# Kernel tuning notes

Measured on AMD Instinct MI355X. Metric: run time of the kernel, lower is better.

The kernel has to match this reference:

```python
import jax, jax.numpy as jnp
import numpy as np

EMBED_DIM = 128
HIDDEN_DIM = 512
NUM_LAYERS = 2
LATENT_DIM = 128
VOCAB = 2048
BATCH = 4096
NEG = -1.0e9  # matches torch masked fill value -1e9
TEMPERATURE = 1.0  # generate() skips the divide when temperature == 1.0


def _gru_cell(x, h, w_ih, w_hh, b_ih, b_hh):
    # PyTorch GRU cell, gate order (r, z, n)
    gi = x @ w_ih.T + b_ih          # [B, 3H]
    gh = h @ w_hh.T + b_hh          # [B, 3H]
    i_r, i_z, i_n = jnp.split(gi, 3, axis=-1)
    h_r, h_z, h_n = jnp.split(gh, 3, axis=-1)
    r = jax.nn.sigmoid(i_r + h_r)
    u = jax.nn.sigmoid(i_z + h_z)
    n = jnp.tanh(i_n + r * h_n)
    return (1.0 - u) * n + u * h


def setup_inputs() -> dict:
    key = jax.random.key(0)
    ks = jax.random.split(key, 16)

    def unif(k, shape, fan):
        bound = 1.0 / np.sqrt(fan)
        return jax.random.uniform(k, shape, jnp.float32, -bound, bound)

    embed = jax.random.normal(ks[0], (VOCAB, EMBED_DIM), jnp.float32)
    embed = embed.at[0].set(0.0)  # padding_idx = 0

    return dict(
        z=jax.random.normal(ks[1], (BATCH, LATENT_DIM), jnp.float32),
        embed=embed,
        w_lh=unif(ks[2], (NUM_LAYERS * HIDDEN_DIM, LATENT_DIM), LATENT_DIM),
        b_lh=unif(ks[3], (NUM_LAYERS * HIDDEN_DIM,), LATENT_DIM),
        w_ih0=unif(ks[4], (3 * HIDDEN_DIM, EMBED_DIM), HIDDEN_DIM),
        w_hh0=unif(ks[5], (3 * HIDDEN_DIM, HIDDEN_DIM), HIDDEN_DIM),
        b_ih0=unif(ks[6], (3 * HIDDEN_DIM,), HIDDEN_DIM),
        b_hh0=unif(ks[7], (3 * HIDDEN_DIM,), HIDDEN_DIM),
        w_ih1=unif(ks[8], (3 * HIDDEN_DIM, HIDDEN_DIM), HIDDEN_DIM),
        w_hh1=unif(ks[9], (3 * HIDDEN_DIM, HIDDEN_DIM), HIDDEN_DIM),
        b_ih1=unif(ks[10], (3 * HIDDEN_DIM,), HIDDEN_DIM),
        b_hh1=unif(ks[11], (3 * HIDDEN_DIM,), HIDDEN_DIM),
        w_out=unif(ks[12], (VOCAB, HIDDEN_DIM), HIDDEN_DIM),
        b_out=unif(ks[13], (VOCAB,), HIDDEN_DIM),
        bos_idx=1, eos_idx=2, pad_idx=0,
        max_len=64, top_k=40, min_generation_length=20,
    )


def reference(z, embed, w_lh, b_lh, w_ih0, w_hh0, b_ih0, b_hh0,
              w_ih1, w_hh1, b_ih1, b_hh1, w_out, b_out,
              bos_idx, eos_idx, pad_idx, max_len, top_k, min_generation_length):
    B = z.shape[0]
    V = w_out.shape[0]
    H = w_hh0.shape[1]
    eff_min = max(0, min(int(min_generation_length), max(0, max_len - 2)))

    # latent -> initial hidden state [L, B, H]
    h = jnp.tanh(z @ w_lh.T + b_lh).reshape(B, NUM_LAYERS, H).transpose(1, 0, 2)
    rows = jnp.arange(B)[:, None]

    def step(carry, t):
        h, cur, finished, key = carry
        key, sk = jax.random.split(key)
        x = embed[cur]                                   # [B, E]
        h0 = _gru_cell(x, h[0], w_ih0, w_hh0, b_ih0, b_hh0)
        h1 = _gru_cell(h0, h[1], w_ih1, w_hh1, b_ih1, b_hh1)
        logits = h1 @ w_out.T + b_out                    # [B, V]
        logits = logits.at[:, bos_idx].set(NEG).at[:, pad_idx].set(NEG)
        # block EOS until min_generation_length real tokens emitted
        logits = jnp.where((t - 1) < eff_min, logits.at[:, eos_idx].set(NEG), logits)
        if TEMPERATURE != 1.0:
            logits = logits / max(TEMPERATURE, 1e-6)
        if 0 < top_k < V:
            tv, ti = jax.lax.top_k(logits, top_k)
            logits = jnp.full_like(logits, NEG).at[rows, ti].set(tv)
        # multinomial over softmax(logits) == categorical on logits
        nxt = jax.random.categorical(sk, logits).astype(jnp.int32)
        nxt = jnp.where(finished, pad_idx, nxt)
        finished = finished | (nxt == eos_idx)
        return (jnp.stack([h0, h1]), nxt, finished, key), nxt

    init = (h,
            jnp.full((B,), bos_idx, jnp.int32),
            jnp.zeros((B,), dtype=bool),
            jax.random.key(1))
    _, toks = jax.lax.scan(step, init, jnp.arange(1, max_len))  # toks: [max_len-1, B]
    return jnp.concatenate(
        [jnp.full((B, 1), bos_idx, jnp.int32), toks.T.astype(jnp.int32)], axis=1)
```

## Files before the change

kernel.cpp:

```cpp
#include <hip/hip_runtime.h>
#include <cstdint>
#include <cstddef>

#ifndef PARTITIONABLE
#define PARTITIONABLE 1
#endif

namespace {
constexpr int kBatch  = 4096;
constexpr int kEmb    = 128;
constexpr int kHid    = 512;
constexpr int kVoc    = 2048;
constexpr int kMaxLen = 64;
constexpr int kTopK   = 40;
constexpr int kBos = 1, kEos = 2, kPad = 0;
constexpr int kEffMin = 20;
constexpr float kNeg  = -1.0e9f;
constexpr float kTiny = 1.17549435082228751e-38f;
}

typedef __bf16 bf16x8 __attribute__((ext_vector_type(8)));
typedef float  f32x4  __attribute__((ext_vector_type(4)));

__host__ __device__ inline void tf2x32(uint32_t k0, uint32_t k1,
                                       uint32_t x0, uint32_t x1,
                                       uint32_t& o0, uint32_t& o1) {
  uint32_t ks0 = k0, ks1 = k1, ks2 = k0 ^ k1 ^ 0x1BD11BDAu;
  x0 += ks0; x1 += ks1;
#define TFR(r) { x0 += x1; x1 = (x1 << (r)) | (x1 >> (32 - (r))); x1 ^= x0; }
  TFR(13) TFR(15) TFR(26) TFR(6)   x0 += ks1; x1 += ks2 + 1u;
  TFR(17) TFR(29) TFR(16) TFR(24)  x0 += ks2; x1 += ks0 + 2u;
  TFR(13) TFR(15) TFR(26) TFR(6)   x0 += ks0; x1 += ks1 + 3u;
  TFR(17) TFR(29) TFR(16) TFR(24)  x0 += ks1; x1 += ks2 + 4u;
  TFR(13) TFR(15) TFR(26) TFR(6)   x0 += ks2; x1 += ks0 + 5u;
#undef TFR
  o0 = x0; o1 = x1;
}

__device__ __forceinline__ float xla_tanh(float x) {
  float ax = fabsf(x);
  float xc = fminf(fmaxf(x, -9.0f), 9.0f);
  float x2 = __fmul_rn(xc, xc);
  float num = -2.76076847742355e-16f;
  num = __fadd_rn(__fmul_rn(x2, num), 2.00018790482477e-13f);
  num = __fadd_rn(__fmul_rn(x2, num), -8.60467152213735e-11f);
  num = __fadd_rn(__fmul_rn(x2, num), 5.12229709037114e-08f);
  num = __fadd_rn(__fmul_rn(x2, num), 1.48572235717979e-05f);
  num = __fadd_rn(__fmul_rn(x2, num), 6.37261928875436e-04f);
  num = __fadd_rn(__fmul_rn(x2, num), 4.89352455891786e-03f);
  num = __fmul_rn(xc, num);
  float den = 1.19825839466702e-06f;
  den = __fadd_rn(__fmul_rn(x2, den), 1.18534705686654e-04f);
  den = __fadd_rn(__fmul_rn(x2, den), 2.26843463243900e-03f);
  den = __fadd_rn(__fmul_rn(x2, den), 4.89352518554385e-03f);
  return (ax < 4.0e-04f) ? x : __fdiv_rn(num, den);
}

__device__ __forceinline__ float xla_sigmoid(float x) {
  return __fdiv_rn(1.0f, __fadd_rn(1.0f, expf(-x)));
}

__device__ __forceinline__ void gl_lds16(const void* g, void* l) {
  __builtin_amdgcn_global_load_lds(
      (const __attribute__((address_space(1))) void*)g,
      (__attribute__((address_space(3))) void*)l, 16, 0, 0);
}

__device__ __forceinline__ void split3(float a, __bf16& a0, __bf16& a1, __bf16& a2) {
  a0 = (__bf16)a;
  float r1 = __fsub_rn(a, (float)a0);
  a1 = (__bf16)r1;
  float r2 = __fsub_rn(r1, (float)a1);
  a2 = (__bf16)r2;
}

__device__ __forceinline__ float gru_h(float gir, float giz, float gin,
                                       float ghr, float ghz, float ghn,
                                       float hold) {
  float r = xla_sigmoid(__fadd_rn(gir, ghr));
  float u = xla_sigmoid(__fadd_rn(giz, ghz));
  float n = xla_tanh(__fadd_rn(gin, __fmul_rn(r, ghn)));
  float t1 = __fmul_rn(__fsub_rn(1.0f, u), n);
  float t2 = __fmul_rn(u, hold);
  return __fadd_rn(t1, t2);
}

#define MFMA9(c, A0_, A1_, A2_, B0_, B1_, B2_) do {                          \
    c = __builtin_amdgcn_mfma_f32_16x16x32_bf16(A2_, B2_, c, 0, 0, 0);       \
    c = __builtin_amdgcn_mfma_f32_16x16x32_bf16(A2_, B1_, c, 0, 0, 0);       \
    c = __builtin_amdgcn_mfma_f32_16x16x32_bf16(A1_, B2_, c, 0, 0, 0);       \
    c = __builtin_amdgcn_mfma_f32_16x16x32_bf16(A2_, B0_, c, 0, 0, 0);       \
    c = __builtin_amdgcn_mfma_f32_16x16x32_bf16(A1_, B1_, c, 0, 0, 0);       \
    c = __builtin_amdgcn_mfma_f32_16x16x32_bf16(A0_, B2_, c, 0, 0, 0);       \
    c = __builtin_amdgcn_mfma_f32_16x16x32_bf16(A1_, B0_, c, 0, 0, 0);       \
    c = __builtin_amdgcn_mfma_f32_16x16x32_bf16(A0_, B1_, c, 0, 0, 0);       \
    c = __builtin_amdgcn_mfma_f32_16x16x32_bf16(A0_, B0_, c, 0, 0, 0);       \
  } while (0)

template <int ACT>
__global__ __launch_bounds__(256) void gemm2(
    const float* __restrict__ A0, const float* __restrict__ B0,
    const float* __restrict__ bias0, float* __restrict__ C0,
    const float* __restrict__ A1, const float* __restrict__ B1,
    const float* __restrict__ bias1, float* __restrict__ C1,
    int lda, int ldb, int ldc, int K) {
  __shared__ __attribute__((aligned(16))) float As[2][128 * 16];
  __shared__ __attribute__((aligned(16))) float Bs[2][16 * 128];

  const float* A    = blockIdx.z ? A1 : A0;
  const float* Bt   = blockIdx.z ? B1 : B0;
  const float* bias = blockIdx.z ? bias1 : bias0;
  float*       C    = blockIdx.z ? C1 : C0;

  const int tid = threadIdx.x;
  const int w = tid >> 6, l = tid & 63;
  const int bm = blockIdx.y * 128;
  const int bn = blockIdx.x * 128;
  const int tx = tid & 15, ty = tid >> 4;
  const int t3 = ty & 3;

  const int arow  = w * 16 + (l >> 2);
  const int agran = (l & 3) ^ ((l >> 2) & 3);
  const float* pA = A + (size_t)(bm + arow) * lda + agran * 4;
  const int bk = w * 2 + (l >> 5);
  const int bnc = (l & 31) * 4;
  const float* pB = Bt + (size_t)bk * ldb + bn + bnc;

  float acc[8][8];
#pragma unroll
  for (int i = 0; i < 8; ++i)
#pragma unroll
    for (int j = 0; j < 8; ++j) acc[i][j] = 0.0f;

  const int nt = K >> 4;
  gl_lds16(pA,            &As[0][w * 256]);
  gl_lds16(pA + 64 * lda, &As[0][(4 + w) * 256]);
  gl_lds16(pB,            &Bs[0][w * 256]);
  gl_lds16(pB + (size_t)8 * ldb, &Bs[0][(4 + w) * 256]);
  __syncthreads();

  for (int t = 0; t < nt; ++t) {
    const int cur = t & 1;
    if (t + 1 < nt) {
      const float* qA = pA + (t + 1) * 16;
      const float* qB = pB + (size_t)(t + 1) * 16 * ldb;
      gl_lds16(qA,            &As[cur ^ 1][w * 256]);
      gl_lds16(qA + 64 * lda, &As[cur ^ 1][(4 + w) * 256]);
      gl_lds16(qB,            &Bs[cur ^ 1][w * 256]);
      gl_lds16(qB + (size_t)8 * ldb, &Bs[cur ^ 1][(4 + w) * 256]);
    }
    const float* as = As[cur];
    const float* bs = Bs[cur];
#pragma unroll
    for (int g = 0; g < 4; ++g) {
      float4 bv0[4], bv1[4];
#pragma unroll
      for (int q = 0; q < 4; ++q) {
        bv0[q] = *(const float4*)&bs[(g * 4 + q) * 128 + tx * 4];
        bv1[q] = *(const float4*)&bs[(g * 4 + q) * 128 + 64 + tx * 4];
      }
#pragma unroll
      for (int ii = 0; ii < 8; ++ii) {
        float4 a = *(const float4*)&as[(ty + 16 * ii) * 16 + ((g ^ t3) * 4)];
        float ak[4] = {a.x, a.y, a.z, a.w};
#pragma unroll
        for (int q = 0; q < 4; ++q) {
          const float av_ = ak[q];
          const float4 b0 = bv0[q], b1 = bv1[q];
          acc[ii][0] += av_ * b0.x; acc[ii][1] += av_ * b0.y;
          acc[ii][2] += av_ * b0.z; acc[ii][3] += av_ * b0.w;
          acc[ii][4] += av_ * b1.x; acc[ii][5] += av_ * b1.y;
          acc[ii][6] += av_ * b1.z; acc[ii][7] += av_ * b1.w;
        }
      }
    }
    __syncthreads();
  }

  const int c0 = bn + tx * 4, c1 = bn + 64 + tx * 4;
  const float4 bs0 = *(const float4*)&bias[c0];
  const float4 bs1 = *(const float4*)&bias[c1];
#pragma unroll
  for (int ii = 0; ii < 8; ++ii) {
    const int r = bm + ty + 16 * ii;
    float4 o0, o1;
    o0.x = acc[ii][0] + bs0.x; o0.y = acc[ii][1] + bs0.y;
    o0.z = acc[ii][2] + bs0.z; o0.w = acc[ii][3] + bs0.w;
    o1.x = acc[ii][4] + bs1.x; o1.y = acc[ii][5] + bs1.y;
    o1.z = acc[ii][6] + bs1.z; o1.w = acc[ii][7] + bs1.w;
    if (ACT == 1) {
      o0.x = xla_tanh(o0.x); o0.y = xla_tanh(o0.y);
      o0.z = xla_tanh(o0.z); o0.w = xla_tanh(o0.w);
      o1.x = xla_tanh(o1.x); o1.y = xla_tanh(o1.y);
      o1.z = xla_tanh(o1.z); o1.w = xla_tanh(o1.w);
    }
    *(float4*)(C + (size_t)r * ldc + c0) = o0;
    *(float4*)(C + (size_t)r * ldc + c1) = o1;
  }
}

struct GemmArgs {
  const __bf16 *a0, *a1, *a2;
  const __bf16 *b0, *b1, *b2;
  const float* bias;
  float* c;
};

__global__ __launch_bounds__(256, 3) void gemm_mx3(
    GemmArgs g0, GemmArgs g1, int N) {
  __shared__ __attribute__((aligned(16))) __bf16 lds[6 * 4096];

  const GemmArgs g = blockIdx.z ? g1 : g0;
  const int tid = threadIdx.x;
  const int nwg = gridDim.x * gridDim.y;
  const int lin = blockIdx.y * gridDim.x + blockIdx.x;
  const int swz = (lin & 7) * (nwg >> 3) + (lin >> 3);
  const int bm = (swz / gridDim.x) * 128;
  const int bn = (swz % gridDim.x) * 128;
  const int lane = tid & 63;
  const int w  = tid >> 6;
  const int wm = w & 1;
  const int wn = w >> 1;
  const int l15 = lane & 15;
  const int kge = (lane >> 4) * 8;

  const int srow = tid >> 2;
  const int sge  = (tid & 3) * 8;
  const __bf16* tp[6];
  tp[0] = g.a0 + (size_t)(bm + srow) * 512 + sge;
  tp[1] = g.a1 + (size_t)(bm + srow) * 512 + sge;
  tp[2] = g.a2 + (size_t)(bm + srow) * 512 + sge;
  tp[3] = g.b0 + (size_t)(bn + srow) * 512 + sge;
  tp[4] = g.b1 + (size_t)(bn + srow) * 512 + sge;
  tp[5] = g.b2 + (size_t)(bn + srow) * 512 + sge;

  int aoff[4], boff[4];
#pragma unroll
  for (int i = 0; i < 4; ++i) {
    aoff[i] = (wm * 64 + i * 16 + l15) * 32 + kge;
    boff[i] = (wn * 64 + i * 16 + l15) * 32 + kge;
  }

  f32x4 acc[4][4] = {};

  for (int s = 0; s < 16; ++s) {
    const int k0 = s * 32;
#pragma unroll
    for (int p = 0; p < 6; ++p) {
      gl_lds16(tp[p] + k0,                    &lds[p * 4096 + w * 512]);
      gl_lds16(tp[p] + (size_t)64 * 512 + k0, &lds[p * 4096 + 2048 + w * 512]);
    }
    __syncthreads();

    bf16x8 Af[3][4];
#pragma unroll
    for (int mi = 0; mi < 4; ++mi) {
      Af[0][mi] = *(const bf16x8*)&lds[0 * 4096 + aoff[mi]];
      Af[1][mi] = *(const bf16x8*)&lds[1 * 4096 + aoff[mi]];
      Af[2][mi] = *(const bf16x8*)&lds[2 * 4096 + aoff[mi]];
    }
#pragma unroll
    for (int nj = 0; nj < 4; ++nj) {
      bf16x8 B0 = *(const bf16x8*)&lds[3 * 4096 + boff[nj]];
      bf16x8 B1 = *(const bf16x8*)&lds[4 * 4096 + boff[nj]];
      bf16x8 B2 = *(const bf16x8*)&lds[5 * 4096 + boff[nj]];
#pragma unroll
      for (int mi = 0; mi < 4; ++mi) {
        f32x4 c = acc[mi][nj];
        MFMA9(c, Af[0][mi], Af[1][mi], Af[2][mi], B0, B1, B2);
        acc[mi][nj] = c;
      }
    }
    __syncthreads();
  }

#pragma unroll
  for (int mi = 0; mi < 4; ++mi) {
    const int row0 = bm + wm * 64 + mi * 16 + (lane >> 4) * 4;
#pragma unroll
    for (int nj = 0; nj < 4; ++nj) {
      const int col = bn + wn * 64 + nj * 16 + l15;
      const float bv = g.bias[col];
      f32x4 v = acc[mi][nj];
#pragma unroll
      for (int r = 0; r < 4; ++r)
        g.c[(size_t)(row0 + r) * N + col] = v[r] + bv;
    }
  }
}

__global__ __launch_bounds__(256, 2) void gemm_gru0(
    const __bf16* __restrict__ a0, const __bf16* __restrict__ a1,
    const __bf16* __restrict__ a2,
    const __bf16* __restrict__ wb0, const __bf16* __restrict__ wb1,
    const __bf16* __restrict__ wb2,
    const float* __restrict__ bias, const float* __restrict__ Eih0,
    const int* __restrict__ curTok,
    __bf16* __restrict__ q0, __bf16* __restrict__ q1,
    __bf16* __restrict__ q2) {
  __shared__ __attribute__((aligned(16))) __bf16 As[3][4096];
  __shared__ __attribute__((aligned(16))) __bf16 Bs[9][1024];

  const int tid = threadIdx.x;
  const int nwg = gridDim.x * gridDim.y;
  const int lin = blockIdx.y * gridDim.x + blockIdx.x;
  const int swz = (lin & 7) * (nwg >> 3) + (lin >> 3);
  const int bm = (swz / gridDim.x) * 128;
  const int bn = (swz % gridDim.x) * 32;
  const int lane = tid & 63;
  const int w  = tid >> 6;
  const int wm = w & 1;
  const int wn = w >> 1;
  const int l15 = lane & 15;
  const int kge = (lane >> 4) * 8;

  const int srow = tid >> 2;
  const int sge  = (tid & 3) * 8;
  const __bf16* tpA[3];
  tpA[0] = a0 + (size_t)(bm + srow) * 512 + sge;
  tpA[1] = a1 + (size_t)(bm + srow) * 512 + sge;
  tpA[2] = a2 + (size_t)(bm + srow) * 512 + sge;

  const int bcol = lane >> 2;
  const int bge  = (lane & 3) * 8;

  int aoff[4];
#pragma unroll
  for (int i = 0; i < 4; ++i)
    aoff[i] = (wm * 64 + i * 16 + l15) * 32 + kge;
  const int boff = (wn * 16 + l15) * 32 + kge;

  f32x4 acc[3][4] = {};

  for (int s = 0; s < 16; ++s) {
    const int k0 = s * 32;
#pragma unroll
    for (int p = 0; p < 3; ++p) {
      gl_lds16(tpA[p] + k0,                    &As[p][w * 512]);
      gl_lds16(tpA[p] + (size_t)64 * 512 + k0, &As[p][2048 + w * 512]);
    }
    for (int qq = w; qq < 9; qq += 4) {
      const int gg = qq / 3, pp = qq - gg * 3;
      const __bf16* wp = (pp == 0) ? wb0 : (pp == 1) ? wb1 : wb2;
      const __bf16* src =
          wp + (size_t)(gg * 512 + bn + bcol) * 512 + bge + k0;
      gl_lds16(src,                     &Bs[qq][0]);
      gl_lds16(src + (size_t)16 * 512,  &Bs[qq][512]);
    }
    __syncthreads();

    bf16x8 Af[3][4];
#pragma unroll
    for (int mi = 0; mi < 4; ++mi) {
      Af[0][mi] = *(const bf16x8*)&As[0][aoff[mi]];
      Af[1][mi] = *(const bf16x8*)&As[1][aoff[mi]];
      Af[2][mi] = *(const bf16x8*)&As[2][aoff[mi]];
    }
#pragma unroll
    for (int gg = 0; gg < 3; ++gg) {
      bf16x8 B0 = *(const bf16x8*)&Bs[gg * 3 + 0][boff];
      bf16x8 B1 = *(const bf16x8*)&Bs[gg * 3 + 1][boff];
      bf16x8 B2 = *(const bf16x8*)&Bs[gg * 3 + 2][boff];
#pragma unroll
      for (int mi = 0; mi < 4; ++mi) {
        f32x4 c = acc[gg][mi];
        MFMA9(c, Af[0][mi], Af[1][mi], Af[2][mi], B0, B1, B2);
        acc[gg][mi] = c;
      }
    }
    __syncthreads();
  }

  const int col = bn + wn * 16 + l15;
  const float bvr = bias[col];
  const float bvz = bias[512 + col];
  const float bvn = bias[1024 + col];
#pragma unroll
  for (int mi = 0; mi < 4; ++mi) {
    const int row0 = bm + wm * 64 + mi * 16 + (lane >> 4) * 4;
#pragma unroll
    for (int rr = 0; rr < 4; ++rr) {
      const int row = row0 + rr;
      const int tok = curTok[row];
      const float* e = Eih0 + (size_t)tok * 1536;
      const size_t idx = (size_t)row * 512 + col;
      float hold = __fadd_rn(__fadd_rn((float)a0[idx], (float)a1[idx]),
                             (float)a2[idx]);
      float hnew = gru_h(e[col], e[512 + col], e[1024 + col],
                         acc[0][mi][rr] + bvr, acc[1][mi][rr] + bvz,
                         acc[2][mi][rr] + bvn, hold);
      __bf16 s0, s1, s2;
      split3(hnew, s0, s1, s2);
      q0[idx] = s0; q1[idx] = s1; q2[idx] = s2;
    }
  }
}

__global__ __launch_bounds__(256, 2) void gemm_gru1(
    const __bf16* __restrict__ x0, const __bf16* __restrict__ x1,
    const __bf16* __restrict__ x2,
    const __bf16* __restrict__ wi0, const __bf16* __restrict__ wi1,
    const __bf16* __restrict__ wi2,
    const __bf16* __restrict__ wh0, const __bf16* __restrict__ wh1,
    const __bf16* __restrict__ wh2,
    const float* __restrict__ bias_i, const float* __restrict__ bias_h,
    const __bf16* __restrict__ hi0, const __bf16* __restrict__ hi1,
    const __bf16* __restrict__ hi2,
    __bf16* __restrict__ ho0, __bf16* __restrict__ ho1,
    __bf16* __restrict__ ho2) {
  __shared__ __attribute__((aligned(16))) __bf16 As[3][4096];
  __shared__ __attribute__((aligned(16))) __bf16 Bs[9][1024];

  const int tid = threadIdx.x;
  const int nwg = gridDim.x * gridDim.y;
  const int lin = blockIdx.y * gridDim.x + blockIdx.x;
  const int swz = (lin & 7) * (nwg >> 3) + (lin >> 3);
  const int bm = (swz / gridDim.x) * 128;
  const int bn = (swz % gridDim.x) * 32;
  const int lane = tid & 63;
  const int w  = tid >> 6;
  const int wm = w & 1;
  const int wn = w >> 1;
  const int l15 = lane & 15;
  const int kge = (lane >> 4) * 8;

  const int srow = tid >> 2;
  const int sge  = (tid & 3) * 8;
  const __bf16* tpX[3];
  tpX[0] = x0 + (size_t)(bm + srow) * 512 + sge;
  tpX[1] = x1 + (size_t)(bm + srow) * 512 + sge;
  tpX[2] = x2 + (size_t)(bm + srow) * 512 + sge;
  const __bf16* tpH[3];
  tpH[0] = hi0 + (size_t)(bm + srow) * 512 + sge;
  tpH[1] = hi1 + (size_t)(bm + srow) * 512 + sge;
  tpH[2] = hi2 + (size_t)(bm + srow) * 512 + sge;

  const int bcol = lane >> 2;
  const int bge  = (lane & 3) * 8;

  int aoff[4];
#pragma unroll
  for (int i = 0; i < 4; ++i)
    aoff[i] = (wm * 64 + i * 16 + l15) * 32 + kge;
  const int boff = (wn * 16 + l15) * 32 + kge;

  f32x4 acci[3][4] = {};
  f32x4 acch[3][4] = {};

  for (int s = 0; s < 16; ++s) {
    const int k0 = s * 32;
#pragma unroll
    for (int p = 0; p < 3; ++p) {
      gl_lds16(tpX[p] + k0,                    &As[p][w * 512]);
      gl_lds16(tpX[p] + (size_t)64 * 512 + k0, &As[p][2048 + w * 512]);
    }
    for (int qq = w; qq < 9; qq += 4) {
      const int gg = qq / 3, pp = qq - gg * 3;
      const __bf16* wp = (pp == 0) ? wi0 : (pp == 1) ? wi1 : wi2;
      const __bf16* src = wp + (size_t)(gg * 512 + bn + bcol) * 512 + bge + k0;
      gl_lds16(src,                    &Bs[qq][0]);
      gl_lds16(src + (size_t)16 * 512, &Bs[qq][512]);
    }
    __syncthreads();
    {
      bf16x8 Af[3][4];
#pragma unroll
      for (int mi = 0; mi < 4; ++mi) {
        Af[0][mi] = *(const bf16x8*)&As[0][aoff[mi]];
        Af[1][mi] = *(const bf16x8*)&As[1][aoff[mi]];
        Af[2][mi] = *(const bf16x8*)&As[2][aoff[mi]];
      }
#pragma unroll
      for (int gg = 0; gg < 3; ++gg) {
        bf16x8 B0 = *(const bf16x8*)&Bs[gg * 3 + 0][boff];
        bf16x8 B1 = *(const bf16x8*)&Bs[gg * 3 + 1][boff];
        bf16x8 B2 = *(const bf16x8*)&Bs[gg * 3 + 2][boff];
#pragma unroll
        for (int mi = 0; mi < 4; ++mi) {
          f32x4 c = acci[gg][mi];
          MFMA9(c, Af[0][mi], Af[1][mi], Af[2][mi], B0, B1, B2);
          acci[gg][mi] = c;
        }
      }
    }
    __syncthreads();
#pragma unroll
    for (int p = 0; p < 3; ++p) {
      gl_lds16(tpH[p] + k0,                    &As[p][w * 512]);
      gl_lds16(tpH[p] + (size_t)64 * 512 + k0, &As[p][2048 + w * 512]);
    }
    for (int qq = w; qq < 9; qq += 4) {
      const int gg = qq / 3, pp = qq - gg * 3;
      const __bf16* wp = (pp == 0) ? wh0 : (pp == 1) ? wh1 : wh2;
      const __bf16* src = wp + (size_t)(gg * 512 + bn + bcol) * 512 + bge + k0;
      gl_lds16(src,                    &Bs[qq][0]);
      gl_lds16(src + (size_t)16 * 512, &Bs[qq][512]);
    }
    __syncthreads();
    {
      bf16x8 Hf[3][4];
#pragma unroll
      for (int mi = 0; mi < 4; ++mi) {
        Hf[0][mi] = *(const bf16x8*)&As[0][aoff[mi]];
        Hf[1][mi] = *(const bf16x8*)&As[1][aoff[mi]];
        Hf[2][mi] = *(const bf16x8*)&As[2][aoff[mi]];
      }
#pragma unroll
      for (int gg = 0; gg < 3; ++gg) {
        bf16x8 B0 = *(const bf16x8*)&Bs[gg * 3 + 0][boff];
        bf16x8 B1 = *(const bf16x8*)&Bs[gg * 3 + 1][boff];
        bf16x8 B2 = *(const bf16x8*)&Bs[gg * 3 + 2][boff];
#pragma unroll
        for (int mi = 0; mi < 4; ++mi) {
          f32x4 c = acch[gg][mi];
          MFMA9(c, Hf[0][mi], Hf[1][mi], Hf[2][mi], B0, B1, B2);
          acch[gg][mi] = c;
        }
      }
    }
    __syncthreads();
  }

  const int col = bn + wn * 16 + l15;
  const float bir = bias_i[col];
  const float biz = bias_i[512 + col];
  const float bin = bias_i[1024 + col];
  const float bhr = bias_h[col];
  const float bhz = bias_h[512 + col];
  const float bhn = bias_h[1024 + col];
#pragma unroll
  for (int mi = 0; mi < 4; ++mi) {
    const int row0 = bm + wm * 64 + mi * 16 + (lane >> 4) * 4;
#pragma unroll
    for (int rr = 0; rr < 4; ++rr) {
      const int row = row0 + rr;
      const size_t idx = (size_t)row * 512 + col;
      float hold = __fadd_rn(__fadd_rn((float)hi0[idx], (float)hi1[idx]),
                             (float)hi2[idx]);
      float hnew = gru_h(acci[0][mi][rr] + bir, acci[1][mi][rr] + biz,
                         acci[2][mi][rr] + bin,
                         acch[0][mi][rr] + bhr, acch[1][mi][rr] + bhz,
                         acch[2][mi][rr] + bhn, hold);
      __bf16 s0, s1, s2;
      split3(hnew, s0, s1, s2);
      ho0[idx] = s0; ho1[idx] = s1; ho2[idx] = s2;
    }
  }
}

__global__ __launch_bounds__(256) void k_split(
    const float* __restrict__ in, __bf16* __restrict__ p0,
    __bf16* __restrict__ p1, __bf16* __restrict__ p2, int total) {
  int i = blockIdx.x * 256 + threadIdx.x;
  if (i >= total) return;
  __bf16 a0, a1, a2;
  split3(in[i], a0, a1, a2);
  p0[i] = a0; p1[i] = a1; p2[i] = a2;
}

__global__ __launch_bounds__(256) void k_transpose(
    const float* __restrict__ in, float* __restrict__ out, int R, int C) {
  __shared__ float tile[32][33];
  int c0 = blockIdx.x * 32, r0 = blockIdx.y * 32;
  int x = threadIdx.x, y0 = threadIdx.y;
  for (int i = y0; i < 32; i += 8) {
    int r = r0 + i, c = c0 + x;
    tile[i][x] = (r < R && c < C) ? in[(size_t)r * C + c] : 0.0f;
  }
  __syncthreads();
  for (int i = y0; i < 32; i += 8) {
    int orow = c0 + i, oc = r0 + x;
    if (orow < C && oc < R) out[(size_t)orow * R + oc] = tile[x][i];
  }
}

__global__ __launch_bounds__(256) void k_sample(
    const float* __restrict__ logits, int* __restrict__ cur,
    int* __restrict__ finished, int* __restrict__ outTok,
    int t, uint32_t sk0, uint32_t sk1) {
  const int row = blockIdx.x;
  const int tid = threadIdx.x;
  __shared__ float sl[kVoc];
  __shared__ uint32_t skeys[kVoc];
  __shared__ int  cnt[256];
  __shared__ int  sfx[257];
  __shared__ int  wtot[4];
  __shared__ uint32_t sPrefix;
  __shared__ int  sNeed;
  __shared__ float redf[4];
  __shared__ int   redix[4];

  const float* lp = logits + (size_t)row * kVoc;
  for (int c = tid; c < kVoc; c += 256) {
    float v = lp[c];
    if (c == kBos || c == kPad) v = kNeg;
    if (c == kEos && t < 1 + kEffMin) v = kNeg;
    sl[c] = v;
    uint32_t u = __float_as_uint(v);
    skeys[c] = u ^ ((u >> 31) ? 0xFFFFFFFFu : 0x80000000u);
  }
  __syncthreads();

  uint32_t prefix = 0u;
  int need = kTopK;
  const int lane = tid & 63, wv = tid >> 6;
  for (int by = 3; by >= 0; --by) {
    cnt[tid] = 0;
    __syncthreads();
    const int sh = by * 8;
    const uint32_t hiMask = (by == 3) ? 0u : (0xFFFFFFFFu << (sh + 8));
    for (int c = tid; c < kVoc; c += 256) {
      uint32_t k = skeys[c];
      if ((k & hiMask) == prefix) atomicAdd(&cnt[(k >> sh) & 255], 1);
    }
    __syncthreads();
    int val = cnt[tid];
#pragma unroll
    for (int off = 1; off < 64; off <<= 1) {
      int other = __shfl_down(val, off, 64);
      if (lane + off < 64) val += other;
    }
    int wt = __shfl(val, 0, 64);
    if (lane == 0) wtot[wv] = wt;
    __syncthreads();
    int tail = 0;
    for (int u = wv + 1; u < 4; ++u) tail += wtot[u];
    sfx[tid] = val + tail;
    if (tid == 0) sfx[256] = 0;
    __syncthreads();
    if (sfx[tid] >= need && sfx[tid + 1] < need) {
      sPrefix = prefix | ((uint32_t)tid << sh);
      sNeed = need - sfx[tid + 1];
    }
    __syncthreads();
    prefix = sPrefix;
    need = sNeed;
    __syncthreads();
  }

  float best = -3.4e38f; int bidx = kVoc;
  for (int c = tid; c < kVoc; c += 256) {
    if (skeys[c] >= prefix) {
      uint32_t idx = (uint32_t)row * (uint32_t)kVoc + (uint32_t)c;
      uint32_t w1, w2, bits;
#if PARTITIONABLE
      tf2x32(sk0, sk1, 0u, idx, w1, w2);
      bits = w1 ^ w2;
#else
      const uint32_t HH = (uint32_t)((uint64_t)kBatch * kVoc / 2);
      if (idx < HH) { tf2x32(sk0, sk1, idx, idx + HH, w1, w2); bits = w1; }
      else          { tf2x32(sk0, sk1, idx - HH, idx, w1, w2); bits = w2; }
#endif
      uint32_t fb = (bits >> 9) | 0x3f800000u;
      float uf = __fsub_rn(__uint_as_float(fb), 1.0f);
      if (uf == 0.0f) uf = kTiny;
      float g = -logf(-logf(uf));
      float tot = __fadd_rn(g, sl[c]);
      if (tot > best || (tot == best && c < bidx)) { best = tot; bidx = c; }
    }
  }
#pragma unroll
  for (int off = 32; off; off >>= 1) {
    float ov = __shfl_down(best, off, 64);
    int   oi = __shfl_down(bidx, off, 64);
    if (ov > best || (ov == best && oi < bidx)) { best = ov; bidx = oi; }
  }
  if ((tid & 63) == 0) { redf[tid >> 6] = best; redix[tid >> 6] = bidx; }
  __syncthreads();
  if (tid == 0) {
    for (int w = 1; w < 4; ++w) {
      if (redf[w] > best || (redf[w] == best && redix[w] < bidx)) {
        best = redf[w]; bidx = redix[w];
      }
    }
    int fin = finished[row];
    int nxt = fin ? kPad : bidx;
    outTok[(size_t)row * kMaxLen + t] = nxt;
    cur[row] = nxt;
    finished[row] = fin | (nxt == kEos);
  }
}

__global__ __launch_bounds__(256) void k_init(int* cur, int* finished, int* outTok) {
  int i = blockIdx.x * 256 + threadIdx.x;
  if (i < kBatch) {
    cur[i] = kBos;
    finished[i] = 0;
    outTok[(size_t)i * kMaxLen] = kBos;
  }
}

extern "C" void kernel_launch(void* const* d_in, const int* in_sizes, int n_in,
                              void* d_out, int out_size, void* d_ws, size_t ws_size,
                              hipStream_t stream) {
  (void)in_sizes; (void)n_in; (void)out_size; (void)ws_size;
  const float* z      = (const float*)d_in[0];
  const float* embed  = (const float*)d_in[1];
  const float* w_lh   = (const float*)d_in[2];
  const float* b_lh   = (const float*)d_in[3];
  const float* w_ih0  = (const float*)d_in[4];
  const float* w_hh0  = (const float*)d_in[5];
  const float* b_ih0  = (const float*)d_in[6];
  const float* b_hh0  = (const float*)d_in[7];
  const float* w_ih1  = (const float*)d_in[8];
  const float* w_hh1  = (const float*)d_in[9];
  const float* b_ih1  = (const float*)d_in[10];
  const float* b_hh1  = (const float*)d_in[11];
  const float* w_out  = (const float*)d_in[12];
  const float* b_out  = (const float*)d_in[13];
  int* out = (int*)d_out;

  char* base = (char*)d_ws;
  int* curTok   = (int*)base;
  int* finished = curTok + kBatch;
  __bf16* q = (__bf16*)(base + 32768);
  __bf16* whh0[3]; __bf16* wih1[3]; __bf16* whh1[3]; __bf16* wout[3];
  for (int i = 0; i < 3; ++i) { whh0[i] = q; q += (size_t)1536 * 512; }
  for (int i = 0; i < 3; ++i) { wih1[i] = q; q += (size_t)1536 * 512; }
  for (int i = 0; i < 3; ++i) { whh1[i] = q; q += (size_t)1536 * 512; }
  for (int i = 0; i < 3; ++i) { wout[i] = q; q += (size_t)2048 * 512; }
  __bf16* hs0A[3]; __bf16* hs1A[3];
  for (int i = 0; i < 3; ++i) { hs0A[i] = q; q += (size_t)kBatch * kHid; }
  for (int i = 0; i < 3; ++i) { hs1A[i] = q; q += (size_t)kBatch * kHid; }
  float* f = (float*)q;
  float* Eih0 = f; f += (size_t)kVoc * 1536;
  float* ghA  = f; f += (size_t)kBatch * 1536;
  float* gi1  = f; f += (size_t)kBatch * 1536;
  float* logits = ghA;
  float* wt_ih0 = ghA;
  float* wt_lh  = ghA + (size_t)128 * 1536;
  float* h0tmp  = gi1;
  float* h1tmp  = gi1 + (size_t)kBatch * kHid;
  __bf16* hs0B[3];
  { __bf16* hb = (__bf16*)f;
    for (int i = 0; i < 3; ++i) { hs0B[i] = hb; hb += (size_t)kBatch * kHid; } }
  __bf16* hs1B[3];
  {
    __bf16* hb = (__bf16*)(gi1 + (size_t)kBatch * kHid);
    for (int i = 0; i < 3; ++i) { hs1B[i] = hb; hb += (size_t)kBatch * kHid; } }

  dim3 blk(256);
  dim3 tblk(32, 8);

  k_transpose<<<dim3(4, 48), tblk, 0, stream>>>(w_ih0, wt_ih0, 1536, 128);
  k_transpose<<<dim3(4, 32), tblk, 0, stream>>>(w_lh,  wt_lh,  1024, 128);
  k_split<<<dim3(1536 * 512 / 256), blk, 0, stream>>>(w_hh0, whh0[0], whh0[1], whh0[2], 1536 * 512);
  k_split<<<dim3(1536 * 512 / 256), blk, 0, stream>>>(w_ih1, wih1[0], wih1[1], wih1[2], 1536 * 512);
  k_split<<<dim3(1536 * 512 / 256), blk, 0, stream>>>(w_hh1, whh1[0], whh1[1], whh1[2], 1536 * 512);
  k_split<<<dim3(2048 * 512 / 256), blk, 0, stream>>>(w_out, wout[0], wout[1], wout[2], 2048 * 512);

  gemm2<0><<<dim3(12, 16, 1), blk, 0, stream>>>(
      embed, wt_ih0, b_ih0, Eih0, embed, wt_ih0, b_ih0, Eih0,
      kEmb, 1536, 1536, kEmb);
  gemm2<1><<<dim3(4, 32, 2), blk, 0, stream>>>(
      z, wt_lh,       b_lh,       h0tmp,
      z, wt_lh + 512, b_lh + 512, h1tmp,
      kEmb, 1024, kHid, kEmb);
  k_split<<<dim3(kBatch * kHid / 256), blk, 0, stream>>>(h0tmp, hs0A[0], hs0A[1], hs0A[2], kBatch * kHid);
  k_split<<<dim3(kBatch * kHid / 256), blk, 0, stream>>>(h1tmp, hs1A[0], hs1A[1], hs1A[2], kBatch * kHid);
  k_init<<<dim3((kBatch + 255) / 256), blk, 0, stream>>>(curTok, finished, out);

  uint32_t key0 = 0u, key1 = 1u;
  for (int t = 1; t < kMaxLen; ++t) {
    uint32_t nk0, nk1, s0, s1;
#if PARTITIONABLE
    tf2x32(key0, key1, 0u, 0u, nk0, nk1);
    tf2x32(key0, key1, 0u, 1u, s0, s1);
#else
    uint32_t a0, b0w, a1, b1w;
    tf2x32(key0, key1, 0u, 2u, a0, b0w);
    tf2x32(key0, key1, 1u, 3u, a1, b1w);
    nk0 = a0; nk1 = a1; s0 = b0w; s1 = b1w;
#endif
    __bf16** h0in  = (t & 1) ? hs0A : hs0B;
    __bf16** h0out = (t & 1) ? hs0B : hs0A;
    __bf16** h1in  = (t & 1) ? hs1A : hs1B;
    __bf16** h1out = (t & 1) ? hs1B : hs1A;

    gemm_gru0<<<dim3(16, 32), blk, 0, stream>>>(
        h0in[0], h0in[1], h0in[2], whh0[0], whh0[1], whh0[2],
        b_hh0, Eih0, curTok, h0out[0], h0out[1], h0out[2]);

    gemm_gru1<<<dim3(16, 32), blk, 0, stream>>>(
        h0out[0], h0out[1], h0out[2],
        wih1[0], wih1[1], wih1[2],
        whh1[0], whh1[1], whh1[2],
        b_ih1, b_hh1,
        h1in[0], h1in[1], h1in[2],
        h1out[0], h1out[1], h1out[2]);

    GemmArgs gla{h1out[0], h1out[1], h1out[2], wout[0], wout[1], wout[2], b_out, logits};
    gemm_mx3<<<dim3(16, 32, 1), blk, 0, stream>>>(gla, gla, 2048);
    k_sample<<<dim3(kBatch), blk, 0, stream>>>(logits, curTok, finished, out, t, s0, s1);

    key0 = nk0; key1 = nk1;
  }
}
```

Measured before the change: 15.89 ms.

## Merge input and hidden GEMM phases in GRU layer-1 kernel, load H directly to registers

```diff
diff --git a/kernel.cpp b/kernel.cpp
--- a/kernel.cpp
+++ b/kernel.cpp
@@ -409,7 +409,7 @@
     __bf16* __restrict__ ho0, __bf16* __restrict__ ho1,
     __bf16* __restrict__ ho2) {
   __shared__ __attribute__((aligned(16))) __bf16 As[3][4096];
-  __shared__ __attribute__((aligned(16))) __bf16 Bs[9][1024];
+  __shared__ __attribute__((aligned(16))) __bf16 Bs[18][1024];
 
   const int tid = threadIdx.x;
   const int nwg = gridDim.x * gridDim.y;
@@ -430,10 +430,11 @@
   tpX[0] = x0 + (size_t)(bm + srow) * 512 + sge;
   tpX[1] = x1 + (size_t)(bm + srow) * 512 + sge;
   tpX[2] = x2 + (size_t)(bm + srow) * 512 + sge;
-  const __bf16* tpH[3];
-  tpH[0] = hi0 + (size_t)(bm + srow) * 512 + sge;
-  tpH[1] = hi1 + (size_t)(bm + srow) * 512 + sge;
-  tpH[2] = hi2 + (size_t)(bm + srow) * 512 + sge;
+
+  const __bf16* aH[3];
+  aH[0] = hi0 + (size_t)(bm + wm * 64 + l15) * 512 + kge;
+  aH[1] = hi1 + (size_t)(bm + wm * 64 + l15) * 512 + kge;
+  aH[2] = hi2 + (size_t)(bm + wm * 64 + l15) * 512 + kge;
 
   const int bcol = lane >> 2;
   const int bge  = (lane & 3) * 8;
@@ -447,6 +448,9 @@
   f32x4 acci[3][4] = {};
   f32x4 acch[3][4] = {};
 
+  const __bf16* wis[3] = {wi0, wi1, wi2};
+  const __bf16* whs[3] = {wh0, wh1, wh2};
+
   for (int s = 0; s < 16; ++s) {
     const int k0 = s * 32;
 #pragma unroll
@@ -454,68 +458,51 @@
       gl_lds16(tpX[p] + k0,                    &As[p][w * 512]);
       gl_lds16(tpX[p] + (size_t)64 * 512 + k0, &As[p][2048 + w * 512]);
     }
-    for (int qq = w; qq < 9; qq += 4) {
-      const int gg = qq / 3, pp = qq - gg * 3;
-      const __bf16* wp = (pp == 0) ? wi0 : (pp == 1) ? wi1 : wi2;
+    for (int qq = w; qq < 18; qq += 4) {
+      const int wset = qq / 9;
+      const int gg = (qq - wset * 9) / 3, pp = qq - wset * 9 - gg * 3;
+      const __bf16* wp = wset ? whs[pp] : wis[pp];
       const __bf16* src = wp + (size_t)(gg * 512 + bn + bcol) * 512 + bge + k0;
       gl_lds16(src,                    &Bs[qq][0]);
       gl_lds16(src + (size_t)16 * 512, &Bs[qq][512]);
     }
-    __syncthreads();
-    {
-      bf16x8 Af[3][4];
+    bf16x8 Hf[3][4];
+#pragma unroll
+    for (int p = 0; p < 3; ++p)
+#pragma unroll
+      for (int mi = 0; mi < 4; ++mi)
+        Hf[p][mi] = *(const bf16x8*)(aH[p] + (size_t)mi * 16 * 512 + k0);
+    __syncthreads();
+
+    bf16x8 Af[3][4];
+#pragma unroll
+    for (int mi = 0; mi < 4; ++mi) {
+      Af[0][mi] = *(const bf16x8*)&As[0][aoff[mi]];
+      Af[1][mi] = *(const bf16x8*)&As[1][aoff[mi]];
+      Af[2][mi] = *(const bf16x8*)&As[2][aoff[mi]];
+    }
+#pragma unroll
+    for (int gg = 0; gg < 3; ++gg) {
+      bf16x8 B0 = *(const bf16x8*)&Bs[gg * 3 + 0][boff];
+      bf16x8 B1 = *(const bf16x8*)&Bs[gg * 3 + 1][boff];
+      bf16x8 B2 = *(const bf16x8*)&Bs[gg * 3 + 2][boff];
 #pragma unroll
       for (int mi = 0; mi < 4; ++mi) {
-        Af[0][mi] = *(const bf16x8*)&As[0][aoff[mi]];
-        Af[1][mi] = *(const bf16x8*)&As[1][aoff[mi]];
-        Af[2][mi] = *(const bf16x8*)&As[2][aoff[mi]];
+        f32x4 c = acci[gg][mi];
+        MFMA9(c, Af[0][mi], Af[1][mi], Af[2][mi], B0, B1, B2);
+        acci[gg][mi] = c;
       }
-#pragma unroll
-      for (int gg = 0; gg < 3; ++gg) {
-        bf16x8 B0 = *(const bf16x8*)&Bs[gg * 3 + 0][boff];
-        bf16x8 B1 = *(const bf16x8*)&Bs[gg * 3 + 1][boff];
-        bf16x8 B2 = *(const bf16x8*)&Bs[gg * 3 + 2][boff];
-#pragma unroll
-        for (int mi = 0; mi < 4; ++mi) {
-          f32x4 c = acci[gg][mi];
-          MFMA9(c, Af[0][mi], Af[1][mi], Af[2][mi], B0, B1, B2);
-          acci[gg][mi] = c;
-        }
-      }
-    }
-    __syncthreads();
-#pragma unroll
-    for (int p = 0; p < 3; ++p) {
-      gl_lds16(tpH[p] + k0,                    &As[p][w * 512]);
-      gl_lds16(tpH[p] + (size_t)64 * 512 + k0, &As[p][2048 + w * 512]);
-    }
-    for (int qq = w; qq < 9; qq += 4) {
-      const int gg = qq / 3, pp = qq - gg * 3;
-      const __bf16* wp = (pp == 0) ? wh0 : (pp == 1) ? wh1 : wh2;
-      const __bf16* src = wp + (size_t)(gg * 512 + bn + bcol) * 512 + bge + k0;
-      gl_lds16(src,                    &Bs[qq][0]);
-      gl_lds16(src + (size_t)16 * 512, &Bs[qq][512]);
-    }
-    __syncthreads();
-    {
-      bf16x8 Hf[3][4];
+    }
+#pragma unroll
+    for (int gg = 0; gg < 3; ++gg) {
+      bf16x8 B0 = *(const bf16x8*)&Bs[9 + gg * 3 + 0][boff];
+      bf16x8 B1 = *(const bf16x8*)&Bs[9 + gg * 3 + 1][boff];
+      bf16x8 B2 = *(const bf16x8*)&Bs[9 + gg * 3 + 2][boff];
 #pragma unroll
       for (int mi = 0; mi < 4; ++mi) {
-        Hf[0][mi] = *(const bf16x8*)&As[0][aoff[mi]];
-        Hf[1][mi] = *(const bf16x8*)&As[1][aoff[mi]];
-        Hf[2][mi] = *(const bf16x8*)&As[2][aoff[mi]];
-      }
-#pragma unroll
-      for (int gg = 0; gg < 3; ++gg) {
-        bf16x8 B0 = *(const bf16x8*)&Bs[gg * 3 + 0][boff];
-        bf16x8 B1 = *(const bf16x8*)&Bs[gg * 3 + 1][boff];
-        bf16x8 B2 = *(const bf16x8*)&Bs[gg * 3 + 2][boff];
-#pragma unroll
-        for (int mi = 0; mi < 4; ++mi) {
-          f32x4 c = acch[gg][mi];
-          MFMA9(c, Hf[0][mi], Hf[1][mi], Hf[2][mi], B0, B1, B2);
-          acch[gg][mi] = c;
-        }
+        f32x4 c = acch[gg][mi];
+        MFMA9(c, Hf[0][mi], Hf[1][mi], Hf[2][mi], B0, B1, B2);
+        acch[gg][mi] = c;
       }
     }
     __syncthreads();
@@ -735,8 +722,7 @@
   { __bf16* hb = (__bf16*)f;
     for (int i = 0; i < 3; ++i) { hs0B[i] = hb; hb += (size_t)kBatch * kHid; } }
   __bf16* hs1B[3];
-  {
-    __bf16* hb = (__bf16*)(gi1 + (size_t)kBatch * kHid);
+  { __bf16* hb = (__bf16*)(gi1 + (size_t)kBatch * kHid);
     for (int i = 0; i < 3; ++i) { hs1B[i] = hb; hb += (size_t)kBatch * kHid; } }
 
   dim3 blk(256);
```

Measured after the change: 16.60 ms. 1.05x slower.
